# Optimization experiments

Hardware: AMD Instinct MI355X
Metric: run time of the kernel (lower is better)

Reference implementation:

```python
import jax, jax.numpy as jnp
import numpy as np

C = 128   # channels
C4 = C // 4

def setup_inputs() -> dict:
    key = jax.random.key(0)
    k1, k2, k3, k4, k5 = jax.random.split(key, 5)
    B, N = 16, 2048
    x_h = jax.random.normal(k1, (B, C, N), dtype=jnp.float32)
    x_o = jax.random.normal(k2, (B, C, N), dtype=jnp.float32)
    # q_conv and k_conv share the SAME weight (tied in __init__), bias=False
    w_qk = jax.random.normal(k3, (C4, C), dtype=jnp.float32) * (1.0 / np.sqrt(C))
    # v_conv: Conv1d(C, C, 1) with bias
    w_v = jax.random.normal(k4, (C, C), dtype=jnp.float32) * (1.0 / np.sqrt(C))
    b_v = jax.random.normal(k5, (C,), dtype=jnp.float32) * 0.01
    return {"x_h": x_h, "x_o": x_o, "w_qk": w_qk, "w_v": w_v, "b_v": b_v}

def reference(x_h, x_o, w_qk, w_v, b_v):
    # SA_Layer_1 forward (only layer used by Grasp_Transformer_Last.forward)
    # 1x1 conv == channel matmul
    xh_q = jnp.einsum('dc,bcn->bnd', w_qk, x_h)            # [B, Nh, C4]
    xo_k = jnp.einsum('dc,bcm->bdm', w_qk, x_o)            # [B, C4, No]
    alpha = jnp.einsum('bnd,bdm->bnm', xh_q, xo_k)         # [B, Nh, No]
    # no softmax: normalize by column sums over dim=1 (Nh axis)
    attention = alpha / (1e-9 + jnp.sum(alpha, axis=1, keepdims=True))
    xo_v = jnp.einsum('dc,bcm->bmd', w_v, x_o) + b_v       # [B, No, C]
    x_r = jnp.einsum('bnm,bmd->bnd', attention, xo_v)      # [B, Nh, C]
    x_r = jnp.transpose(x_r, (0, 2, 1))                    # [B, C, Nh]
    return (x_r, attention)
```

## Files before the change

### kernel.cpp

```cpp
#include <hip/hip_runtime.h>

constexpr int NTOK = 2048;
constexpr int CH   = 128;
constexpr int C4   = 32;
constexpr int NB   = 16;

typedef __attribute__((ext_vector_type(8))) __bf16 bf16x8;
typedef __attribute__((ext_vector_type(4))) float  f32x4;

__device__ __forceinline__ unsigned short f2bf(float f) {
  union { float f; unsigned u; } v; v.f = f;
  unsigned r = v.u + 0x7fffu + ((v.u >> 16) & 1u);
  return (unsigned short)(r >> 16);
}
__device__ __forceinline__ float bf2f(unsigned short h) {
  union { unsigned u; float f; } v; v.u = ((unsigned)h) << 16;
  return v.f;
}

__global__ __launch_bounds__(256) void rs_kernel(const float* __restrict__ x_h,
                                                 double* __restrict__ rowsumH) {
  const int lane = threadIdx.x & 63;
  const int c = blockIdx.x * 4 + (threadIdx.x >> 6);
  const int b = blockIdx.y;
  const float* rp = x_h + (size_t)(b * CH + c) * NTOK;
  double s = 0.0;
#pragma unroll
  for (int i = 0; i < 8; ++i) {
    float4 v = *(const float4*)(rp + (lane + 64 * i) * 4);
    s += (double)v.x + (double)v.y + (double)v.z + (double)v.w;
  }
  for (int off = 1; off <= 32; off <<= 1) s += __shfl_xor(s, off);
  if (lane == 0) rowsumH[b * CH + c] = s;
}

__global__ __launch_bounds__(256) void prep_qk(const float* __restrict__ x_h,
                                               const float* __restrict__ x_o,
                                               const float* __restrict__ w_qk,
                                               const double* __restrict__ rowsumH,
                                               float* __restrict__ xhq_f32,
                                               float* __restrict__ xokT_f32,
                                               unsigned short* __restrict__ xhq_hi,
                                               unsigned short* __restrict__ xokT_hi,
                                               unsigned short* __restrict__ xhq_lo,
                                               unsigned short* __restrict__ xokT_lo,
                                               float* __restrict__ inv) {
  const int t = threadIdx.x;
  const int n0 = blockIdx.x * 64;
  const int b = blockIdx.y;
  const int which = blockIdx.z;
  const float* src = which ? x_o : x_h;
  float* dstf = which ? xokT_f32 : xhq_f32;
  unsigned short* dsth = which ? xokT_hi : xhq_hi;
  unsigned short* dstl = which ? xokT_lo : xhq_lo;

  __shared__ float Xt[CH][64];
  __shared__ float Wl[C4][132];
  __shared__ double Sl[C4];
  __shared__ double Pl[CH];

  for (int i = 0; i < 8; ++i) {
    int flat = t + 256 * i;
    int c = flat >> 4, f4 = flat & 15;
    float4 v = *(const float4*)(src + (size_t)(b * CH + c) * NTOK + n0 + f4 * 4);
    *(float4*)&Xt[c][f4 * 4] = v;
  }
  for (int i = 0; i < 4; ++i) {
    int flat = t + 256 * i;
    int d = flat >> 5, f4 = flat & 31;
    float4 v = *(const float4*)(w_qk + d * CH + f4 * 4);
    *(float4*)&Wl[d][f4 * 4] = v;
  }
  __syncthreads();

  const int nb = (t & 15) * 4;
  const int d0 = (t >> 4) * 2;
  float acc[4][2] = {};
#pragma unroll 4
  for (int c = 0; c < CH; ++c) {
    float4 x4 = *(const float4*)&Xt[c][nb];
    float w0 = Wl[d0][c], w1 = Wl[d0 + 1][c];
    acc[0][0] += x4.x * w0; acc[0][1] += x4.x * w1;
    acc[1][0] += x4.y * w0; acc[1][1] += x4.y * w1;
    acc[2][0] += x4.z * w0; acc[2][1] += x4.z * w1;
    acc[3][0] += x4.w * w0; acc[3][1] += x4.w * w1;
  }

  const size_t robase = (size_t)(b * NTOK + n0 + nb);
#pragma unroll
  for (int i = 0; i < 4; ++i) {
    size_t base = (robase + i) * C4 + d0;
    *(float2*)(dstf + base) = make_float2(acc[i][0], acc[i][1]);
    unsigned short h0 = f2bf(acc[i][0]), h1 = f2bf(acc[i][1]);
    *(unsigned*)(dsth + base) = (unsigned)h0 | ((unsigned)h1 << 16);
    unsigned short l0 = f2bf(acc[i][0] - bf2f(h0));
    unsigned short l1 = f2bf(acc[i][1] - bf2f(h1));
    *(unsigned*)(dstl + base) = (unsigned)l0 | ((unsigned)l1 << 16);
  }

  if (which) {
    if (t < C4) {
      double s = 0.0;
      for (int c = 0; c < CH; ++c) s += (double)Wl[t][c] * rowsumH[b * CH + c];
      Sl[t] = s;
    }
    __syncthreads();
    if (t < CH) {
      double p = 0.0;
      for (int d = 0; d < C4; ++d) p += Sl[d] * (double)Wl[d][t];
      Pl[t] = p;
    }
    __syncthreads();
    if (t < 64) {
      double s = 0.0;
      for (int c = 0; c < CH; ++c) s += Pl[c] * (double)Xt[c][t];
      inv[b * NTOK + n0 + t] = (float)(1.0 / (1e-9 + s));
    }
  }
}

__global__ __launch_bounds__(256) void u_kernel(const float* __restrict__ x_o,
                                                const float* __restrict__ xokT_f32,
                                                const float* __restrict__ inv,
                                                float* __restrict__ U4) {
  const int t = threadIdx.x;
  const int c0 = blockIdx.x * 8;
  const int slab = blockIdx.y;
  const int mbase0 = slab * 512;
  const int b = blockIdx.z;
  const int d = t & 31, cl = t >> 5;
  __shared__ float Xs[8][256];
  float acc = 0.f;
  for (int cc = 0; cc < 2; ++cc) {
    const int mb = mbase0 + cc * 256;
    __syncthreads();
    for (int i = 0; i < 2; ++i) {
      int flat = t + 256 * i;
      int row = flat >> 6, f4 = flat & 63;
      float4 xv = *(const float4*)(x_o + (size_t)(b * CH + c0 + row) * NTOK + mb + f4 * 4);
      float4 iv = *(const float4*)(inv + b * NTOK + mb + f4 * 4);
      xv.x *= iv.x; xv.y *= iv.y; xv.z *= iv.z; xv.w *= iv.w;
      *(float4*)&Xs[row][f4 * 4] = xv;
    }
    __syncthreads();
    const float* ap = xokT_f32 + (size_t)(b * NTOK + mb) * C4 + d;
#pragma unroll 4
    for (int mm = 0; mm < 256; mm += 4) {
      float4 xq = *(const float4*)&Xs[cl][mm];
      float a0 = ap[(mm + 0) * C4];
      float a1 = ap[(mm + 1) * C4];
      float a2 = ap[(mm + 2) * C4];
      float a3 = ap[(mm + 3) * C4];
      acc += a0 * xq.x + a1 * xq.y + a2 * xq.z + a3 * xq.w;
    }
  }
  U4[(size_t)((b * 4 + slab) * C4 + d) * CH + c0 + cl] = acc;
}

__global__ __launch_bounds__(256) void t_kernel(const float* __restrict__ U4,
                                                const float* __restrict__ w_v,
                                                const float* __restrict__ b_v,
                                                const float* __restrict__ xokT_f32,
                                                const float* __restrict__ inv,
                                                float* __restrict__ T) {
  const int t = threadIdx.x;
  const int cgrp = blockIdx.x;
  const int b = blockIdx.y;
  const int d = t & 31;
  const int g = t >> 5;
  __shared__ float Wl[16][CH];
  __shared__ float S2s[8][C4];
  {
    const float* kp = xokT_f32 + (size_t)b * NTOK * C4;
    const float* ip = inv + b * NTOK;
    float s = 0.f;
    for (int m = g * 256; m < g * 256 + 256; ++m) s += kp[(size_t)m * C4 + d] * ip[m];
    S2s[g][d] = s;
  }
  for (int i = 0; i < 2; ++i) {
    int flat = t + 256 * i;
    *(float4*)&Wl[0][flat * 4] = *(const float4*)(w_v + (size_t)cgrp * 16 * CH + flat * 4);
  }
  __syncthreads();
  float s2 = 0.f;
#pragma unroll
  for (int gg = 0; gg < 8; ++gg) s2 += S2s[gg][d];
  const int c0 = g * 2;
  float acc0 = 0.f, acc1 = 0.f;
  const float* up = U4 + (size_t)(b * 4 * C4 + d) * CH;
  for (int cp = 0; cp < CH; ++cp) {
    float u = up[cp] + up[C4 * CH + cp] + up[2 * C4 * CH + cp] + up[3 * C4 * CH + cp];
    acc0 += u * Wl[c0][cp];
    acc1 += u * Wl[c0 + 1][cp];
  }
  const int cglob = cgrp * 16 + c0;
  acc0 += s2 * b_v[cglob];
  acc1 += s2 * b_v[cglob + 1];
  *(float2*)(T + (size_t)(b * C4 + d) * CH + cglob) = make_float2(acc0, acc1);
}

__global__ __launch_bounds__(512) void xr_kernel(const float* __restrict__ xhq_f32,
                                                 const float* __restrict__ T,
                                                 float* __restrict__ out0) {
  const int t = threadIdx.x;
  const int nl = t & 127;
  const int half = t >> 7;
  const int n = blockIdx.x * 128 + nl;
  const int b = blockIdx.y;
  __shared__ float Tl[CH][36];
  for (int i = 0; i < 8; ++i) {
    int flat = t + 512 * i;
    int d = flat >> 7, c = flat & 127;
    Tl[c][d] = T[(size_t)b * C4 * CH + flat];
  }
  __syncthreads();
  float xq[C4];
  const float* qp = xhq_f32 + (size_t)(b * NTOK + n) * C4;
#pragma unroll
  for (int i = 0; i < 8; ++i) {
    float4 v = *(const float4*)(qp + i * 4);
    xq[i * 4] = v.x; xq[i * 4 + 1] = v.y; xq[i * 4 + 2] = v.z; xq[i * 4 + 3] = v.w;
  }
  float* op = out0 + (size_t)b * CH * NTOK + n;
  for (int c = half * 32; c < half * 32 + 32; ++c) {
    float acc = 0.f;
#pragma unroll
    for (int dd = 0; dd < C4; dd += 4) {
      float4 tv = *(const float4*)&Tl[c][dd];
      acc += xq[dd] * tv.x + xq[dd + 1] * tv.y + xq[dd + 2] * tv.z + xq[dd + 3] * tv.w;
    }
    op[(size_t)c * NTOK] = acc;
  }
}

__global__ __launch_bounds__(256) void attn_kernel(const unsigned short* __restrict__ xhq_hi,
                                                   const unsigned short* __restrict__ xhq_lo,
                                                   const unsigned short* __restrict__ xokT_hi,
                                                   const unsigned short* __restrict__ xokT_lo,
                                                   const float* __restrict__ inv,
                                                   float* __restrict__ out1) {
  const int t = threadIdx.x;
  const int wave = t >> 6, lane = t & 63;
  const int quad = lane >> 4, l16 = lane & 15;
  const int m0 = blockIdx.x * 64;
  const int n0 = blockIdx.y * 64;
  const int b = blockIdx.z;

  __shared__ float tile[64][68];

  const int n = n0 + wave * 16 + l16;
  const size_t abase = (size_t)(b * NTOK + n) * C4 + quad * 8;
  bf16x8 ah = *(const bf16x8*)(const void*)(xhq_hi + abase);
  bf16x8 al = *(const bf16x8*)(const void*)(xhq_lo + abase);

  bf16x8 bh[4], bl[4];
  float invv[4];
#pragma unroll
  for (int tt = 0; tt < 4; ++tt) {
    int m = m0 + tt * 16 + l16;
    size_t bbase = (size_t)(b * NTOK + m) * C4 + quad * 8;
    bh[tt] = *(const bf16x8*)(const void*)(xokT_hi + bbase);
    bl[tt] = *(const bf16x8*)(const void*)(xokT_lo + bbase);
    invv[tt] = inv[b * NTOK + m];
  }

  const int trow = wave * 16 + quad * 4;
#pragma unroll
  for (int tt = 0; tt < 4; ++tt) {
    f32x4 z = {0.f, 0.f, 0.f, 0.f};
    f32x4 acc = __builtin_amdgcn_mfma_f32_16x16x32_bf16(al, bh[tt], z, 0, 0, 0);
    acc = __builtin_amdgcn_mfma_f32_16x16x32_bf16(ah, bl[tt], acc, 0, 0, 0);
    acc = __builtin_amdgcn_mfma_f32_16x16x32_bf16(ah, bh[tt], acc, 0, 0, 0);
#pragma unroll
    for (int r = 0; r < 4; ++r)
      tile[trow + r][tt * 16 + l16] = acc[r] * invv[tt];
  }
  __syncthreads();

  const int g = lane >> 4;
#pragma unroll
  for (int s = 0; s < 4; ++s) {
    const int row = wave * 4 + g + s * 16;
    f32x4 v = *(const f32x4*)&tile[row][l16 * 4];
    float* dst = out1 + ((size_t)(b * NTOK) + n0 + row) * NTOK + m0 + l16 * 4;
    __builtin_nontemporal_store(v, (f32x4*)dst);
  }
}

extern "C" void kernel_launch(void* const* d_in, const int* in_sizes, int n_in,
                              void* d_out, int out_size, void* d_ws, size_t ws_size,
                              hipStream_t stream) {
  (void)in_sizes; (void)n_in; (void)out_size; (void)ws_size;
  const float* x_h  = (const float*)d_in[0];
  const float* x_o  = (const float*)d_in[1];
  const float* w_qk = (const float*)d_in[2];
  const float* w_v  = (const float*)d_in[3];
  const float* b_v  = (const float*)d_in[4];
  float* out0 = (float*)d_out;
  float* out1 = out0 + (size_t)NB * CH * NTOK;

  char* ws = (char*)d_ws;
  float* xhq_f32        = (float*)(ws + 0);
  float* xokT_f32       = (float*)(ws + 4194304);
  unsigned short* xhq_hi  = (unsigned short*)(ws + 8388608);
  unsigned short* xokT_hi = (unsigned short*)(ws + 10485760);
  unsigned short* xhq_lo  = (unsigned short*)(ws + 12582912);
  unsigned short* xokT_lo = (unsigned short*)(ws + 14680064);
  float* inv      = (float*)(ws + 16777216);
  float* U4       = (float*)(ws + 16908288);
  float* T        = (float*)(ws + 17956864);
  double* rowsumH = (double*)(ws + 18219008);

  rs_kernel <<<dim3(32, NB), 256, 0, stream>>>(x_h, rowsumH);
  prep_qk   <<<dim3(32, NB, 2), 256, 0, stream>>>(x_h, x_o, w_qk, rowsumH,
                                                  xhq_f32, xokT_f32,
                                                  xhq_hi, xokT_hi, xhq_lo, xokT_lo, inv);
  u_kernel  <<<dim3(16, 4, NB), 256, 0, stream>>>(x_o, xokT_f32, inv, U4);
  t_kernel  <<<dim3(8, NB), 256, 0, stream>>>(U4, w_v, b_v, xokT_f32, inv, T);
  xr_kernel <<<dim3(16, NB), 512, 0, stream>>>(xhq_f32, T, out0);
  attn_kernel<<<dim3(32, 32, NB), 256, 0, stream>>>(xhq_hi, xhq_lo, xokT_hi, xokT_lo,
                                                    inv, out1);
}
```

Before: 387.1 us.

## Fuse T and xr kernels, move S2 reduction into prep, restructure u_kernel

Moves the S2 (key times inv column sum) reduction into prep_qk using shared and global atomics, so t_kernel no longer rescans xokT. Merges t_kernel and xr_kernel into one txr_kernel that recomputes a 16-channel slice of T per block and writes out0 with nontemporal stores, which removes a launch and the T round trip. u_kernel now splits the m range across thread groups with an 8-channel register accumulation and a shared-memory reduction. The cost is redundant T computation across the four n-slabs, an added memset, and float atomics whose summation order is nondeterministic.

Result: no change. 385.6 us (-0.4%).

```diff
diff --git a/kernel.cpp b/kernel.cpp
--- a/kernel.cpp
+++ b/kernel.cpp
@@ -44,7 +44,8 @@
                                                unsigned short* __restrict__ xokT_hi,
                                                unsigned short* __restrict__ xhq_lo,
                                                unsigned short* __restrict__ xokT_lo,
-                                               float* __restrict__ inv) {
+                                               float* __restrict__ inv,
+                                               float* __restrict__ S2g) {
   const int t = threadIdx.x;
   const int n0 = blockIdx.x * 64;
   const int b = blockIdx.y;
@@ -58,6 +59,8 @@
   __shared__ float Wl[C4][132];
   __shared__ double Sl[C4];
   __shared__ double Pl[CH];
+  __shared__ float invl[64];
+  __shared__ float S2blk[C4];
 
   for (int i = 0; i < 8; ++i) {
     int flat = t + 256 * i;
@@ -104,6 +107,7 @@
       for (int c = 0; c < CH; ++c) s += (double)Wl[t][c] * rowsumH[b * CH + c];
       Sl[t] = s;
     }
+    if (t < C4) S2blk[t] = 0.f;
     __syncthreads();
     if (t < CH) {
       double p = 0.0;
@@ -114,8 +118,22 @@
     if (t < 64) {
       double s = 0.0;
       for (int c = 0; c < CH; ++c) s += Pl[c] * (double)Xt[c][t];
-      inv[b * NTOK + n0 + t] = (float)(1.0 / (1e-9 + s));
-    }
+      float ivf = (float)(1.0 / (1e-9 + s));
+      inv[b * NTOK + n0 + t] = ivf;
+      invl[t] = ivf;
+    }
+    __syncthreads();
+    float s0 = 0.f, s1 = 0.f;
+#pragma unroll
+    for (int i = 0; i < 4; ++i) {
+      float iv = invl[nb + i];
+      s0 += acc[i][0] * iv;
+      s1 += acc[i][1] * iv;
+    }
+    atomicAdd(&S2blk[d0], s0);
+    atomicAdd(&S2blk[d0 + 1], s1);
+    __syncthreads();
+    if (t < C4) atomicAdd(&S2g[b * C4 + t], S2blk[t]);
   }
 }
 
@@ -128,9 +146,10 @@
   const int slab = blockIdx.y;
   const int mbase0 = slab * 512;
   const int b = blockIdx.z;
-  const int d = t & 31, cl = t >> 5;
+  const int d = t & 31, g = t >> 5;
   __shared__ float Xs[8][256];
-  float acc = 0.f;
+  __shared__ float Ured[8][8][32];
+  float acc[8] = {};
   for (int cc = 0; cc < 2; ++cc) {
     const int mb = mbase0 + cc * 256;
     __syncthreads();
@@ -143,48 +162,52 @@
       *(float4*)&Xs[row][f4 * 4] = xv;
     }
     __syncthreads();
-    const float* ap = xokT_f32 + (size_t)(b * NTOK + mb) * C4 + d;
-#pragma unroll 4
-    for (int mm = 0; mm < 256; mm += 4) {
-      float4 xq = *(const float4*)&Xs[cl][mm];
-      float a0 = ap[(mm + 0) * C4];
-      float a1 = ap[(mm + 1) * C4];
-      float a2 = ap[(mm + 2) * C4];
-      float a3 = ap[(mm + 3) * C4];
-      acc += a0 * xq.x + a1 * xq.y + a2 * xq.z + a3 * xq.w;
-    }
-  }
-  U4[(size_t)((b * 4 + slab) * C4 + d) * CH + c0 + cl] = acc;
-}
-
-__global__ __launch_bounds__(256) void t_kernel(const float* __restrict__ U4,
-                                                const float* __restrict__ w_v,
-                                                const float* __restrict__ b_v,
-                                                const float* __restrict__ xokT_f32,
-                                                const float* __restrict__ inv,
-                                                float* __restrict__ T) {
+    const float* ap = xokT_f32 + (size_t)(b * NTOK + mb + g * 32) * C4 + d;
+#pragma unroll
+    for (int mm = 0; mm < 32; mm += 4) {
+      float k0 = ap[(mm + 0) * C4];
+      float k1 = ap[(mm + 1) * C4];
+      float k2 = ap[(mm + 2) * C4];
+      float k3 = ap[(mm + 3) * C4];
+#pragma unroll
+      for (int c = 0; c < 8; ++c) {
+        f32x4 xv = *(const f32x4*)&Xs[c][g * 32 + mm];
+        acc[c] += k0 * xv[0] + k1 * xv[1] + k2 * xv[2] + k3 * xv[3];
+      }
+    }
+  }
+#pragma unroll
+  for (int c = 0; c < 8; ++c) Ured[g][c][d] = acc[c];
+  __syncthreads();
+  const int d2 = t & 31, c2 = t >> 5;
+  float s = 0.f;
+#pragma unroll
+  for (int g2 = 0; g2 < 8; ++g2) s += Ured[g2][c2][d2];
+  U4[(size_t)((b * 4 + slab) * C4 + d2) * CH + c0 + c2] = s;
+}
+
+__global__ __launch_bounds__(256) void txr_kernel(const float* __restrict__ U4,
+                                                  const float* __restrict__ w_v,
+                                                  const float* __restrict__ b_v,
+                                                  const float* __restrict__ S2g,
+                                                  const float* __restrict__ xhq_f32,
+                                                  float* __restrict__ out0) {
   const int t = threadIdx.x;
-  const int cgrp = blockIdx.x;
+  const int cgrp  = blockIdx.x & 7;
+  const int nslab = blockIdx.x >> 3;
   const int b = blockIdx.y;
   const int d = t & 31;
   const int g = t >> 5;
   __shared__ float Wl[16][CH];
-  __shared__ float S2s[8][C4];
-  {
-    const float* kp = xokT_f32 + (size_t)b * NTOK * C4;
-    const float* ip = inv + b * NTOK;
-    float s = 0.f;
-    for (int m = g * 256; m < g * 256 + 256; ++m) s += kp[(size_t)m * C4 + d] * ip[m];
-    S2s[g][d] = s;
-  }
+  __shared__ float Tl[16][36];
+
   for (int i = 0; i < 2; ++i) {
     int flat = t + 256 * i;
     *(float4*)&Wl[0][flat * 4] = *(const float4*)(w_v + (size_t)cgrp * 16 * CH + flat * 4);
   }
   __syncthreads();
-  float s2 = 0.f;
-#pragma unroll
-  for (int gg = 0; gg < 8; ++gg) s2 += S2s[gg][d];
+
+  const float s2 = S2g[b * C4 + d];
   const int c0 = g * 2;
   float acc0 = 0.f, acc1 = 0.f;
   const float* up = U4 + (size_t)(b * 4 * C4 + d) * CH;
@@ -194,42 +217,32 @@
     acc1 += u * Wl[c0 + 1][cp];
   }
   const int cglob = cgrp * 16 + c0;
-  acc0 += s2 * b_v[cglob];
-  acc1 += s2 * b_v[cglob + 1];
-  *(float2*)(T + (size_t)(b * C4 + d) * CH + cglob) = make_float2(acc0, acc1);
-}
-
-__global__ __launch_bounds__(512) void xr_kernel(const float* __restrict__ xhq_f32,
-                                                 const float* __restrict__ T,
-                                                 float* __restrict__ out0) {
-  const int t = threadIdx.x;
-  const int nl = t & 127;
-  const int half = t >> 7;
-  const int n = blockIdx.x * 128 + nl;
-  const int b = blockIdx.y;
-  __shared__ float Tl[CH][36];
-  for (int i = 0; i < 8; ++i) {
-    int flat = t + 512 * i;
-    int d = flat >> 7, c = flat & 127;
-    Tl[c][d] = T[(size_t)b * C4 * CH + flat];
-  }
-  __syncthreads();
-  float xq[C4];
-  const float* qp = xhq_f32 + (size_t)(b * NTOK + n) * C4;
-#pragma unroll
-  for (int i = 0; i < 8; ++i) {
-    float4 v = *(const float4*)(qp + i * 4);
-    xq[i * 4] = v.x; xq[i * 4 + 1] = v.y; xq[i * 4 + 2] = v.z; xq[i * 4 + 3] = v.w;
-  }
-  float* op = out0 + (size_t)b * CH * NTOK + n;
-  for (int c = half * 32; c < half * 32 + 32; ++c) {
-    float acc = 0.f;
-#pragma unroll
-    for (int dd = 0; dd < C4; dd += 4) {
-      float4 tv = *(const float4*)&Tl[c][dd];
-      acc += xq[dd] * tv.x + xq[dd + 1] * tv.y + xq[dd + 2] * tv.z + xq[dd + 3] * tv.w;
-    }
-    op[(size_t)c * NTOK] = acc;
+  Tl[c0][d]     = acc0 + s2 * b_v[cglob];
+  Tl[c0 + 1][d] = acc1 + s2 * b_v[cglob + 1];
+  __syncthreads();
+
+  const int nbase = nslab * 512;
+#pragma unroll
+  for (int nn = 0; nn < 2; ++nn) {
+    const int n = nbase + nn * 256 + t;
+    float xq[C4];
+    const float* qp = xhq_f32 + (size_t)(b * NTOK + n) * C4;
+#pragma unroll
+    for (int i = 0; i < 8; ++i) {
+      float4 v = *(const float4*)(qp + i * 4);
+      xq[i * 4] = v.x; xq[i * 4 + 1] = v.y; xq[i * 4 + 2] = v.z; xq[i * 4 + 3] = v.w;
+    }
+    float* op = out0 + (size_t)(b * CH + cgrp * 16) * NTOK + n;
+#pragma unroll
+    for (int c = 0; c < 16; ++c) {
+      float acc = 0.f;
+#pragma unroll
+      for (int dd = 0; dd < C4; dd += 4) {
+        f32x4 tv = *(const f32x4*)&Tl[c][dd];
+        acc += xq[dd] * tv[0] + xq[dd + 1] * tv[1] + xq[dd + 2] * tv[2] + xq[dd + 3] * tv[3];
+      }
+      __builtin_nontemporal_store(acc, op + (size_t)c * NTOK);
+    }
   }
 }
 
@@ -308,16 +321,17 @@
   unsigned short* xokT_lo = (unsigned short*)(ws + 14680064);
   float* inv      = (float*)(ws + 16777216);
   float* U4       = (float*)(ws + 16908288);
-  float* T        = (float*)(ws + 17956864);
-  double* rowsumH = (double*)(ws + 18219008);
-
+  float* S2g      = (float*)(ws + 17956864);
+  double* rowsumH = (double*)(ws + 17959936);
+
+  hipMemsetAsync(S2g, 0, NB * C4 * sizeof(float), stream);
   rs_kernel <<<dim3(32, NB), 256, 0, stream>>>(x_h, rowsumH);
   prep_qk   <<<dim3(32, NB, 2), 256, 0, stream>>>(x_h, x_o, w_qk, rowsumH,
                                                   xhq_f32, xokT_f32,
-                                                  xhq_hi, xokT_hi, xhq_lo, xokT_lo, inv);
+                                                  xhq_hi, xokT_hi, xhq_lo, xokT_lo,
+                                                  inv, S2g);
   u_kernel  <<<dim3(16, 4, NB), 256, 0, stream>>>(x_o, xokT_f32, inv, U4);
-  t_kernel  <<<dim3(8, NB), 256, 0, stream>>>(U4, w_v, b_v, xokT_f32, inv, T);
-  xr_kernel <<<dim3(16, NB), 512, 0, stream>>>(xhq_f32, T, out0);
+  txr_kernel<<<dim3(32, NB), 256, 0, stream>>>(U4, w_v, b_v, S2g, xhq_f32, out0);
   attn_kernel<<<dim3(32, 32, NB), 256, 0, stream>>>(xhq_hi, xhq_lo, xokT_hi, xokT_lo,
                                                     inv, out1);
 }
```
